# Optimization experiments

Hardware: AMD Instinct MI355X
Metric: run time of the kernel (lower is better)

The kernel has to match this reference:

```python
import jax, jax.numpy as jnp
import numpy as np
import math

DIMS = 2560
N_HEADS = 32
ROT_DIM = 32  # partial rotary (Phi-2)
BASE = 10000.0
B, L = 1, 2048


def apply_rope(x, rot_dim=ROT_DIM, base=BASE, offset=0):
    # x: [B, H, L, hd]; rotate first rot_dim features, pass rest through
    Lx = x.shape[2]
    D = rot_dim // 2
    pos = jnp.arange(offset, offset + Lx, dtype=jnp.float32)              # [L]
    freq = jnp.exp(-jnp.arange(D, dtype=jnp.float32) * (math.log(base) / D))  # [D]
    theta = pos[:, None] * freq[None, :]                                   # [L, D]
    cos, sin = jnp.cos(theta), jnp.sin(theta)
    x1 = x[..., :D]
    x2 = x[..., D:rot_dim]
    rx1 = x1 * cos - x2 * sin
    rx2 = x1 * sin + x2 * cos
    return jnp.concatenate([rx1, rx2, x[..., rot_dim:]], axis=-1)


def setup_inputs() -> dict:
    key = jax.random.key(0)
    k1, k2, k3, k4, k5 = jax.random.split(key, 5)
    x = jax.random.normal(k1, (B, L, DIMS), dtype=jnp.float32)
    Wqkv_w = jax.random.normal(k2, (3 * DIMS, DIMS), dtype=jnp.float32) * 0.02
    Wqkv_b = jax.random.normal(k3, (3 * DIMS,), dtype=jnp.float32) * 0.02
    out_w = jax.random.normal(k4, (DIMS, DIMS), dtype=jnp.float32) * 0.02
    out_b = jax.random.normal(k5, (DIMS,), dtype=jnp.float32) * 0.02
    # additive causal mask, broadcast over batch/heads
    mask = jnp.triu(jnp.full((L, L), -1e9, dtype=jnp.float32), k=1)[None, None]
    return {"x": x, "Wqkv_w": Wqkv_w, "Wqkv_b": Wqkv_b,
            "out_w": out_w, "out_b": out_b, "mask": mask}


def reference(x, Wqkv_w, Wqkv_b, out_w, out_b, mask):
    Bx, Lx, _ = x.shape
    hd = DIMS // N_HEADS  # 80
    qkv = x @ Wqkv_w.T + Wqkv_b                          # [B, L, 3*dims]
    q, k, v = jnp.split(qkv, 3, axis=-1)
    def to_heads(t):
        return t.reshape(Bx, Lx, N_HEADS, hd).transpose(0, 2, 1, 3)  # [B,H,L,hd]
    q, k, v = to_heads(q), to_heads(k), to_heads(v)
    q = apply_rope(q)
    k = apply_rope(k)
    scale = 1.0 / math.sqrt(hd)
    scores = scale * jnp.einsum('bhqd,bhkd->bhqk', q, k) + mask  # [B,H,L,L]
    probs = jax.nn.softmax(scores, axis=-1)
    out = jnp.einsum('bhqk,bhkd->bhqd', probs, v)
    out = out.transpose(0, 2, 1, 3).reshape(Bx, Lx, DIMS)
    return out @ out_w.T + out_b
```

## Files before the change

kernel.cpp:

```cpp
#include <hip/hip_runtime.h>
#include <cstdint>
#include <cmath>

typedef __attribute__((ext_vector_type(4))) float f32x4;
typedef __attribute__((ext_vector_type(8))) short s16x8;

#define LOG2E 1.4426950408889634f

__device__ __forceinline__ unsigned short f2bf(float f) {
    unsigned int u = __float_as_uint(f);
    u += 0x7FFFu + ((u >> 16) & 1u);
    return (unsigned short)(u >> 16);
}
__device__ __forceinline__ float bf2f(unsigned short s) {
    return __uint_as_float(((unsigned int)s) << 16);
}

__device__ __forceinline__ void async_copy16(const void* g, void* l) {
    __builtin_amdgcn_global_load_lds(
        (const __attribute__((address_space(1))) unsigned int*)(uintptr_t)g,
        (__attribute__((address_space(3))) unsigned int*)(uintptr_t)l,
        16, 0, 0);
}

__global__ __launch_bounds__(256) void cast_bf16_kernel(const float* __restrict__ in,
                                                        unsigned short* __restrict__ out,
                                                        int n4) {
    int i = blockIdx.x * 256 + threadIdx.x;
    if (i < n4) {
        float4 v = ((const float4*)in)[i];
        ushort4 o;
        o.x = f2bf(v.x); o.y = f2bf(v.y); o.z = f2bf(v.z); o.w = f2bf(v.w);
        ((ushort4*)out)[i] = o;
    }
}

template <bool BF16_OUT>
__global__ __launch_bounds__(256) void gemm_bt(const unsigned short* __restrict__ A,
                                               const unsigned short* __restrict__ B,
                                               const float* __restrict__ bias,
                                               void* __restrict__ Cout,
                                               int M, int N, int K) {
    __shared__ unsigned short As[128 * 64];
    __shared__ unsigned short Bs[128 * 64];
    const int tid  = threadIdx.x;
    const int lane = tid & 63;
    const int wv   = tid >> 6;
    const int m0 = blockIdx.y * 128;
    const int n0 = blockIdx.x * 128;
    const int w_row = (wv >> 1) * 64;
    const int w_col = (wv & 1) * 64;
    const int fr = lane & 15;
    const int fg = lane >> 4;
    const int srow = lane >> 3;
    const int scol = ((lane & 7) ^ srow) * 8;
    const int rofs0 = ((fg ^ (fr & 7))) * 8;
    const int rofs1 = rofs0 ^ 32;

    f32x4 acc[4][4];
    const f32x4 zf = {0.f, 0.f, 0.f, 0.f};
    for (int r = 0; r < 4; ++r)
        for (int c = 0; c < 4; ++c) acc[r][c] = zf;

    const unsigned short* gA = A + (size_t)(m0 + wv * 32 + srow) * K + scol;
    const unsigned short* gB = B + (size_t)(n0 + wv * 32 + srow) * K + scol;

    for (int k0 = 0; k0 < K; k0 += 64) {
        for (int i = 0; i < 4; ++i)
            async_copy16(gA + (size_t)i * 8 * K + k0, &As[(wv * 32 + i * 8) * 64]);
        for (int i = 0; i < 4; ++i)
            async_copy16(gB + (size_t)i * 8 * K + k0, &Bs[(wv * 32 + i * 8) * 64]);
        __syncthreads();
        {
            s16x8 af[4], bf[4];
            for (int r = 0; r < 4; ++r)
                af[r] = *(const s16x8*)&As[(w_row + r * 16 + fr) * 64 + rofs0];
            for (int c = 0; c < 4; ++c)
                bf[c] = *(const s16x8*)&Bs[(w_col + c * 16 + fr) * 64 + rofs0];
            for (int r = 0; r < 4; ++r)
                for (int c = 0; c < 4; ++c)
                    acc[r][c] = __builtin_amdgcn_mfma_f32_16x16x32_bf16(af[r], bf[c], acc[r][c], 0, 0, 0);
        }
        {
            s16x8 af[4], bf[4];
            for (int r = 0; r < 4; ++r)
                af[r] = *(const s16x8*)&As[(w_row + r * 16 + fr) * 64 + rofs1];
            for (int c = 0; c < 4; ++c)
                bf[c] = *(const s16x8*)&Bs[(w_col + c * 16 + fr) * 64 + rofs1];
            for (int r = 0; r < 4; ++r)
                for (int c = 0; c < 4; ++c)
                    acc[r][c] = __builtin_amdgcn_mfma_f32_16x16x32_bf16(af[r], bf[c], acc[r][c], 0, 0, 0);
        }
        __syncthreads();
    }

    const int rb = (lane >> 4) * 4;
    for (int c = 0; c < 4; ++c) {
        int col = n0 + w_col + c * 16 + fr;
        float bv = bias[col];
        for (int r = 0; r < 4; ++r) {
            int row = m0 + w_row + r * 16 + rb;
            for (int q = 0; q < 4; ++q) {
                float v = acc[r][c][q] + bv;
                if constexpr (BF16_OUT)
                    ((unsigned short*)Cout)[(size_t)(row + q) * N + col] = f2bf(v);
                else
                    ((float*)Cout)[(size_t)(row + q) * N + col] = v;
            }
        }
    }
}


#define BAR()   __builtin_amdgcn_s_barrier()
#define VMW(N)  asm volatile("s_waitcnt vmcnt(" #N ")" ::: "memory")

#define STAGE2(gXb, XsBuf, rb, kk) \
    async_copy16(gXb + (size_t)(rb) * K + (kk), (void*)&XsBuf[(rb) * 64])

#define ST_AS0(b, kk) { STAGE2(gAb, As[b], rbA_0, kk);      STAGE2(gAb, As[b], rbA_1, kk); }
#define ST_AS1(b, kk) { STAGE2(gAb, As[b], rbA_0 + 64, kk); STAGE2(gAb, As[b], rbA_1 + 64, kk); }
#define ST_BS0(b, kk) { STAGE2(gBb, Bs[b], rbB_0, kk);      STAGE2(gBb, Bs[b], rbB_1, kk); }
#define ST_BS1(b, kk) { STAGE2(gBb, Bs[b], rbB_0 + 32, kk); STAGE2(gBb, Bs[b], rbB_1 + 32, kk); }

#define READ_A(b, mh) \
    _Pragma("unroll") \
    for (int mm_ = 0; mm_ < 4; ++mm_) { \
        const unsigned short* ap_ = &As[b][(wr * 128 + (mh) * 64 + mm_ * 16 + fr) * 64]; \
        Ar[mm_][0] = *(const s16x8*)(ap_ + rofs0); \
        Ar[mm_][1] = *(const s16x8*)(ap_ + rofs1); \
    }

#define READ_B(b, nh, Brg) \
    _Pragma("unroll") \
    for (int nn_ = 0; nn_ < 2; ++nn_) { \
        const unsigned short* bp_ = &Bs[b][(wc * 64 + (nh) * 32 + nn_ * 16 + fr) * 64]; \
        Brg[nn_][0] = *(const s16x8*)(bp_ + rofs0); \
        Brg[nn_][1] = *(const s16x8*)(bp_ + rofs1); \
    }

#define MFMA_Q(mh, nh, Brg) \
    _Pragma("unroll") \
    for (int mm_ = 0; mm_ < 4; ++mm_) { \
        _Pragma("unroll") \
        for (int nn_ = 0; nn_ < 2; ++nn_) { \
            acc[(mh) * 4 + mm_][(nh) * 2 + nn_] = __builtin_amdgcn_mfma_f32_16x16x32_bf16( \
                Ar[mm_][0], Brg[nn_][0], acc[(mh) * 4 + mm_][(nh) * 2 + nn_], 0, 0, 0); \
            acc[(mh) * 4 + mm_][(nh) * 2 + nn_] = __builtin_amdgcn_mfma_f32_16x16x32_bf16( \
                Ar[mm_][1], Brg[nn_][1], acc[(mh) * 4 + mm_][(nh) * 2 + nn_], 0, 0, 0); \
        } \
    }

#define GROUP(b, t) { \
    int x1_ = (t) + 1; if (x1_ >= ktiles) x1_ -= ktiles; \
    int x2_ = (t) + 2; if (x2_ >= ktiles) x2_ -= ktiles; \
    const int kn1 = x1_ << 6; \
    const int kn2 = x2_ << 6; \
     \
    __builtin_amdgcn_s_setprio(1); MFMA_Q(0, 0, Br0); __builtin_amdgcn_s_setprio(0); \
    VMW(6); \
    READ_B(b, 1, Br1); \
    ST_AS1((b) ^ 1, kn1); \
    BAR(); \
     \
    __builtin_amdgcn_s_setprio(1); MFMA_Q(0, 1, Br1); __builtin_amdgcn_s_setprio(0); \
    VMW(6); \
    READ_A(b, 1); \
    ST_AS0(b, kn2); \
    BAR(); \
     \
    __builtin_amdgcn_s_setprio(1); MFMA_Q(1, 1, Br1); __builtin_amdgcn_s_setprio(0); \
    VMW(6); \
    ST_BS0(b, kn2); \
    BAR(); \
     \
    __builtin_amdgcn_s_setprio(1); MFMA_Q(1, 0, Br0); __builtin_amdgcn_s_setprio(0); \
    VMW(6); \
    READ_A((b) ^ 1, 0); \
    READ_B((b) ^ 1, 0, Br0); \
    ST_BS1(b, kn2); \
    BAR(); \
}

__global__ __launch_bounds__(512, 2) void gemm256_bt(const unsigned short* __restrict__ A,
                                                     const unsigned short* __restrict__ B,
                                                     const float* __restrict__ bias,
                                                     unsigned short* __restrict__ C,
                                                     int M, int N, int K) {
    __shared__ unsigned short As[2][256 * 64];
    __shared__ unsigned short Bs[2][256 * 64];
    const int tid  = threadIdx.x;
    const int lane = tid & 63;
    const int wv   = tid >> 6;
    const int wr   = wv >> 2;
    const int wc   = wv & 3;
    const int j     = blockIdx.x & 7;
    const int local = blockIdx.x >> 3;
    const int strip = 2 * (j & 3) + (local & 1);
    const int panel = (j >> 2) * 15 + (local >> 1);
    const int m0 = strip * 256;
    const int n0 = panel * 256;
    const int fr = lane & 15;
    const int fg = lane >> 4;
    const int rofs0 = (fg ^ (fr & 7)) * 8;
    const int rofs1 = rofs0 ^ 32;
    const int rlane = lane >> 3;
    const int swzc  = ((lane & 7) ^ (rlane & 7)) * 8;
    const int idx0 = wv * 2, idx1 = wv * 2 + 1;
    const int rbA_0 = idx0 * 8 + ((idx0 >= 8) ? 64 : 0);
    const int rbA_1 = idx1 * 8 + ((idx1 >= 8) ? 64 : 0);
    const int rbB_0 = (idx0 >> 2) * 64 + (idx0 & 3) * 8;
    const int rbB_1 = (idx1 >> 2) * 64 + (idx1 & 3) * 8;
    const int ktiles = K >> 6;

    const unsigned short* gAb = A + (size_t)(m0 + rlane) * K + swzc;
    const unsigned short* gBb = B + (size_t)(n0 + rlane) * K + swzc;

    f32x4 acc[8][4];
    const f32x4 zf = {0.f, 0.f, 0.f, 0.f};
#pragma unroll
    for (int i = 0; i < 8; ++i)
#pragma unroll
        for (int jj = 0; jj < 4; ++jj) acc[i][jj] = zf;

    s16x8 Ar[4][2], Br0[2][2], Br1[2][2];

    ST_AS0(0, 0); ST_AS1(0, 0); ST_BS0(0, 0); ST_BS1(0, 0);
    ST_AS0(1, 64); ST_BS0(1, 64); ST_BS1(1, 64);
    VMW(6);
    BAR();
    READ_A(0, 0);
    READ_B(0, 0, Br0);

    const int nit = ktiles >> 1;
    for (int it = 0; it < nit; ++it) {
        GROUP(0, it * 2);
        GROUP(1, it * 2 + 1);
    }

    const int rb = (lane >> 4) * 4;
#pragma unroll
    for (int nn = 0; nn < 4; ++nn) {
        int col = n0 + wc * 64 + nn * 16 + fr;
        float bv = bias[col];
#pragma unroll
        for (int mm = 0; mm < 8; ++mm) {
            int row = m0 + wr * 128 + mm * 16 + rb;
#pragma unroll
            for (int q = 0; q < 4; ++q) {
                float v = acc[mm][nn][q] + bv;
                C[(size_t)(row + q) * N + col] = f2bf(v);
            }
        }
    }
}

__global__ __launch_bounds__(256) void rope_q_kernel(unsigned short* __restrict__ qkv) {
    int g = blockIdx.x * 256 + threadIdx.x;
    int c = g & 1;
    int h = (g >> 1) & 31;
    int p = g >> 6;
    size_t base = (size_t)p * 7680 + h * 80 + c * 8;
    s16x8 x1v = *(const s16x8*)(qkv + base);
    s16x8 x2v = *(const s16x8*)(qkv + base + 16);
    s16x8 o1, o2;
    for (int j = 0; j < 8; ++j) {
        int dp = c * 8 + j;
        float freq = expf(-(float)dp * 0.57564627324851142f);
        float sn, cs;
        sincosf((float)p * freq, &sn, &cs);
        float x1 = bf2f((unsigned short)x1v[j]);
        float x2 = bf2f((unsigned short)x2v[j]);
        o1[j] = (short)f2bf(x1 * cs - x2 * sn);
        o2[j] = (short)f2bf(x1 * sn + x2 * cs);
    }
    *(s16x8*)(qkv + base)      = o1;
    *(s16x8*)(qkv + base + 16) = o2;
}

__global__ __launch_bounds__(256) void rope_pack_k_kernel(const unsigned short* __restrict__ qkv,
                                                          unsigned short* __restrict__ Kp) {
    int g = blockIdx.x * 256 + threadIdx.x;
    int c   = g % 12;
    int h   = (g / 12) & 31;
    int pos = g / 384;
    int d0 = c * 8;
    const unsigned short* kb = qkv + (size_t)pos * 7680 + 2560 + h * 80;
    s16x8 v = {0, 0, 0, 0, 0, 0, 0, 0};
    if (c >= 4) {
        if (d0 < 80) v = *(const s16x8*)(kb + d0);
    } else if (c < 2) {
        s16x8 x1v = *(const s16x8*)(kb + d0);
        s16x8 x2v = *(const s16x8*)(kb + d0 + 16);
        for (int j = 0; j < 8; ++j) {
            int dp = d0 + j;
            float freq = expf(-(float)dp * 0.57564627324851142f);
            float sn, cs;
            sincosf((float)pos * freq, &sn, &cs);
            v[j] = (short)f2bf(bf2f((unsigned short)x1v[j]) * cs -
                               bf2f((unsigned short)x2v[j]) * sn);
        }
    } else {
        s16x8 x1v = *(const s16x8*)(kb + d0 - 16);
        s16x8 x2v = *(const s16x8*)(kb + d0);
        for (int j = 0; j < 8; ++j) {
            int dp = d0 - 16 + j;
            float freq = expf(-(float)dp * 0.57564627324851142f);
            float sn, cs;
            sincosf((float)pos * freq, &sn, &cs);
            v[j] = (short)f2bf(bf2f((unsigned short)x1v[j]) * sn +
                               bf2f((unsigned short)x2v[j]) * cs);
        }
    }
    *(s16x8*)(Kp + (((size_t)h * 64 + (pos >> 5)) * 12 + c) * 256 + (pos & 31) * 8) = v;
}

__global__ __launch_bounds__(256) void pack_v_kernel(const unsigned short* __restrict__ qkv,
                                                     unsigned short* __restrict__ Vp) {
    int h  = blockIdx.x & 31;
    int g64 = blockIdx.x >> 5;
    int k0 = g64 * 64;
    int tid = threadIdx.x;
    for (int ci = tid; ci < 320; ci += 256) {
        int d   = ci % 80;
        int kbl = ci / 80;
        unsigned short tmp[16];
        for (int j = 0; j < 16; ++j)
            tmp[j] = qkv[(size_t)(k0 + kbl * 16 + j) * 7680 + 5120 + h * 80 + d];
        unsigned short* dst = Vp + ((size_t)h * 128 + g64 * 4 + kbl) * 1280 + d * 16;
        *(s16x8*)dst       = *(const s16x8*)&tmp[0];
        *(s16x8*)(dst + 8) = *(const s16x8*)&tmp[8];
    }
}

__global__ __launch_bounds__(256) void flash6_kernel(const unsigned short* __restrict__ qkv,
                                                     const unsigned short* __restrict__ Kp,
                                                     const unsigned short* __restrict__ Vp,
                                                     unsigned short* __restrict__ attn) {
    __shared__ unsigned short Ks[2][3072];
    __shared__ unsigned short Vs[2][2560];
    __shared__ unsigned short Pt[4][640];
    const int tid  = threadIdx.x;
    const int lane = tid & 63;
    const int wv   = tid >> 6;
    const int h  = blockIdx.x & 31;
    const int jj = blockIdx.x >> 5;
    const int fr = lane & 15;
    const int fg = lane >> 4;
    const float k1 = 0.11180339887498949f * LOG2E;

    const int sA  = jj + 16 * wv;
    const int sB  = jj + 112 - 16 * wv;
    const int smA = sA * 16;
    const int smB = sB * 16;
    const int Ublk = (jj + 114) >> 1;

    const s16x8 zs = {0, 0, 0, 0, 0, 0, 0, 0};
    s16x8 qfA[3], qfB[3];
    {
        const unsigned short* qa = qkv + (size_t)(smA + fr) * 7680 + h * 80;
        const unsigned short* qb = qkv + (size_t)(smB + fr) * 7680 + h * 80;
        for (int sd = 0; sd < 3; ++sd) {
            int d = 32 * sd + fg * 8;
            qfA[sd] = (d < 80) ? *(const s16x8*)(qa + d) : zs;
            qfB[sd] = (d < 80) ? *(const s16x8*)(qb + d) : zs;
        }
    }

    f32x4 OA[5], OB[5];
    const f32x4 zf = {0.f, 0.f, 0.f, 0.f};
    for (int t = 0; t < 5; ++t) { OA[t] = zf; OB[t] = zf; }
    float rsA[4] = {0.f, 0.f, 0.f, 0.f};
    float rsB[4] = {0.f, 0.f, 0.f, 0.f};
    unsigned short* Pw = &Pt[wv][0];

    const unsigned short* Kh = Kp + (size_t)h * 196608;
    const unsigned short* Vh = Vp + (size_t)h * 163840;

#define STG1(q, b, uu) { \
    if ((q) < 6) async_copy16(Kh + (size_t)(uu) * 3072 + (q) * 512 + lane * 8, &Ks[b][(q) * 512]); \
    else         async_copy16(Vh + (size_t)(uu) * 2560 + ((q) - 6) * 512 + lane * 8, &Vs[b][((q) - 6) * 512]); }
#define STAGEU(b, uu) { STG1(wv, b, uu); STG1(wv + 4, b, uu); if (wv < 3) STG1(wv + 8, b, uu); }

#define SMX(SA, RS, SM16, K0, PA) { \
    if ((K0) + 32 > (SM16)) { \
        _Pragma("unroll") \
        for (int g = 0; g < 2; ++g) \
            _Pragma("unroll") \
            for (int r = 0; r < 4; ++r) { \
                int key  = (K0) + g * 16 + fr; \
                int qrow = (SM16) + fg * 4 + r; \
                if (key > qrow) SA[g][r] = -1e30f; \
            } \
    } \
    float pr[2][4]; \
    _Pragma("unroll") \
    for (int g = 0; g < 2; ++g) \
        _Pragma("unroll") \
        for (int r = 0; r < 4; ++r) \
            pr[g][r] = __builtin_amdgcn_exp2f(SA[g][r] * k1); \
    _Pragma("unroll") \
    for (int r = 0; r < 4; ++r) RS[r] += pr[0][r] + pr[1][r]; \
    _Pragma("unroll") \
    for (int g = 0; g < 2; ++g) \
        _Pragma("unroll") \
        for (int r = 0; r < 4; ++r) \
            Pw[(fg * 4 + r) * 40 + g * 16 + fr] = \
                (unsigned short)(__float_as_uint(pr[g][r]) >> 16); \
    PA = *(const s16x8*)(Pw + fr * 40 + fg * 8); }

    STAGEU(0, 0);
    __syncthreads();
    int buf = 0;
    for (int u = 0; u < Ublk; ++u) {
        if (u + 1 < Ublk) STAGEU(buf ^ 1, u + 1);
        const int k0 = u * 32;
        const bool actA = (2 * u <= sA);
        const bool actB = (2 * u <= sB);
        if (actB) {
            s16x8 kb[2][3];
#pragma unroll
            for (int g = 0; g < 2; ++g)
#pragma unroll
                for (int sd = 0; sd < 3; ++sd)
                    kb[g][sd] = *(const s16x8*)&Ks[buf][(fg + sd * 4) * 256 + (g * 16 + fr) * 8];
            s16x8 vb[5];
#pragma unroll
            for (int t = 0; t < 5; ++t)
                vb[t] = *(const s16x8*)&Vs[buf][(fg >> 1) * 1280 + t * 256 + fr * 16 + (fg & 1) * 8];

            f32x4 saA[2] = {zf, zf};
            f32x4 saB[2] = {zf, zf};
            __builtin_amdgcn_s_setprio(1);
            if (actA) {
#pragma unroll
                for (int g = 0; g < 2; ++g)
#pragma unroll
                    for (int sd = 0; sd < 3; ++sd)
                        saA[g] = __builtin_amdgcn_mfma_f32_16x16x32_bf16(qfA[sd], kb[g][sd], saA[g], 0, 0, 0);
            }
#pragma unroll
            for (int g = 0; g < 2; ++g)
#pragma unroll
                for (int sd = 0; sd < 3; ++sd)
                    saB[g] = __builtin_amdgcn_mfma_f32_16x16x32_bf16(qfB[sd], kb[g][sd], saB[g], 0, 0, 0);
            __builtin_amdgcn_s_setprio(0);

            s16x8 paA, paB;
            if (actA) SMX(saA, rsA, smA, k0, paA);
            SMX(saB, rsB, smB, k0, paB);

            __builtin_amdgcn_s_setprio(1);
            if (actA) {
#pragma unroll
                for (int t = 0; t < 5; ++t)
                    OA[t] = __builtin_amdgcn_mfma_f32_16x16x32_bf16(paA, vb[t], OA[t], 0, 0, 0);
            }
#pragma unroll
            for (int t = 0; t < 5; ++t)
                OB[t] = __builtin_amdgcn_mfma_f32_16x16x32_bf16(paB, vb[t], OB[t], 0, 0, 0);
            __builtin_amdgcn_s_setprio(0);
        }
        __syncthreads();
        buf ^= 1;
    }
#undef STG1
#undef STAGEU
#undef SMX

#define FIN6(RS, OO, SM16) { \
    _Pragma("unroll") \
    for (int r = 0; r < 4; ++r) { \
        float v = RS[r]; \
        v += __shfl_xor(v, 1); \
        v += __shfl_xor(v, 2); \
        v += __shfl_xor(v, 4); \
        v += __shfl_xor(v, 8); \
        RS[r] = v; \
    } \
    _Pragma("unroll") \
    for (int r = 0; r < 4; ++r) { \
        float rl = 1.0f / RS[r]; \
        int row = (SM16) + fg * 4 + r; \
        _Pragma("unroll") \
        for (int t = 0; t < 5; ++t) \
            attn[(size_t)row * 2560 + h * 80 + t * 16 + fr] = f2bf(OO[t][r] * rl); \
    } }
    FIN6(rsA, OA, smA);
    FIN6(rsB, OB, smB);
#undef FIN6
}

extern "C" void kernel_launch(void* const* d_in, const int* in_sizes, int n_in,
                              void* d_out, int out_size, void* d_ws, size_t ws_size,
                              hipStream_t stream) {
    const float* x    = (const float*)d_in[0];
    const float* wqkv = (const float*)d_in[1];
    const float* bqkv = (const float*)d_in[2];
    const float* outw = (const float*)d_in[3];
    const float* outb = (const float*)d_in[4];

    unsigned short* xb    = (unsigned short*)d_ws;
    unsigned short* wqkvb = xb + (size_t)2048 * 2560;
    unsigned short* Kp    = wqkvb;
    unsigned short* Vp    = wqkvb + (size_t)32 * 2048 * 96;
    unsigned short* outwb = wqkvb + (size_t)7680 * 2560;
    unsigned short* qkvb  = outwb + (size_t)2560 * 2560;
    unsigned short* attnb = qkvb  + (size_t)2048 * 7680;
    float* out = (float*)d_out;

    cast_bf16_kernel<<<2048 * 2560 / 4 / 256, 256, 0, stream>>>(x, xb, 2048 * 2560 / 4);
    cast_bf16_kernel<<<7680 * 2560 / 4 / 256, 256, 0, stream>>>(wqkv, wqkvb, 7680 * 2560 / 4);
    cast_bf16_kernel<<<2560 * 2560 / 4 / 256, 256, 0, stream>>>(outw, outwb, 2560 * 2560 / 4);

    gemm256_bt<<<240, 512, 0, stream>>>(xb, wqkvb, bqkv, qkvb, 2048, 7680, 2560);

    rope_q_kernel<<<2048 * 64 / 256, 256, 0, stream>>>(qkvb);
    rope_pack_k_kernel<<<2048 * 384 / 256, 256, 0, stream>>>(qkvb, Kp);
    pack_v_kernel<<<32 * 32, 256, 0, stream>>>(qkvb, Vp);

    flash6_kernel<<<512, 256, 0, stream>>>(qkvb, Kp, Vp, attnb);

    gemm_bt<false><<<dim3(2560 / 128, 2048 / 128), 256, 0, stream>>>(
        attnb, outwb, outb, (void*)out, 2048, 2560, 2560);
}
```

Measured before the change: 411.2 us.

## Compute transposed QK^T so P feeds PV MFMA from registers without LDS

The flash attention kernel swaps the MFMA operands so the score tile comes out transposed, with each lane holding consecutive keys for one query row. Probabilities can then be packed straight into the bf16 A-operand register instead of going through a per-wave LDS round trip. The V pack kernel permutes key order within each 32-key block to match the new register layout of P. Row sums collapse to one scalar per lane, reduced with cross-group shuffles at the end. This removes LDS writes and reads and their latency from the inner loop, but it depends on the key permutation exactly matching the MFMA fragment layout.

```diff
diff --git a/kernel.cpp b/kernel.cpp
--- a/kernel.cpp
+++ b/kernel.cpp
@@ -4,6 +4,7 @@
 
 typedef __attribute__((ext_vector_type(4))) float f32x4;
 typedef __attribute__((ext_vector_type(8))) short s16x8;
+typedef __attribute__((ext_vector_type(4))) unsigned int u32x4;
 
 #define LOG2E 1.4426950408889634f
 
@@ -325,21 +326,23 @@
         int d   = ci % 80;
         int kbl = ci / 80;
         unsigned short tmp[16];
-        for (int j = 0; j < 16; ++j)
-            tmp[j] = qkv[(size_t)(k0 + kbl * 16 + j) * 7680 + 5120 + h * 80 + d];
+        for (int j = 0; j < 16; ++j) {
+            int s  = (kbl & 1) * 16 + j;
+            int kt = ((s & 7) >> 2) * 16 + (s >> 3) * 4 + (s & 3);
+            tmp[j] = qkv[(size_t)(k0 + (kbl >> 1) * 32 + kt) * 7680 + 5120 + h * 80 + d];
+        }
         unsigned short* dst = Vp + ((size_t)h * 128 + g64 * 4 + kbl) * 1280 + d * 16;
         *(s16x8*)dst       = *(const s16x8*)&tmp[0];
         *(s16x8*)(dst + 8) = *(const s16x8*)&tmp[8];
     }
 }
 
-__global__ __launch_bounds__(256) void flash6_kernel(const unsigned short* __restrict__ qkv,
+__global__ __launch_bounds__(256) void flash8_kernel(const unsigned short* __restrict__ qkv,
                                                      const unsigned short* __restrict__ Kp,
                                                      const unsigned short* __restrict__ Vp,
                                                      unsigned short* __restrict__ attn) {
     __shared__ unsigned short Ks[2][3072];
     __shared__ unsigned short Vs[2][2560];
-    __shared__ unsigned short Pt[4][640];
     const int tid  = threadIdx.x;
     const int lane = tid & 63;
     const int wv   = tid >> 6;
@@ -370,9 +373,7 @@
     f32x4 OA[5], OB[5];
     const f32x4 zf = {0.f, 0.f, 0.f, 0.f};
     for (int t = 0; t < 5; ++t) { OA[t] = zf; OB[t] = zf; }
-    float rsA[4] = {0.f, 0.f, 0.f, 0.f};
-    float rsB[4] = {0.f, 0.f, 0.f, 0.f};
-    unsigned short* Pw = &Pt[wv][0];
+    float rsA = 0.f, rsB = 0.f;
 
     const unsigned short* Kh = Kp + (size_t)h * 196608;
     const unsigned short* Vh = Vp + (size_t)h * 163840;
@@ -382,14 +383,14 @@
     else         async_copy16(Vh + (size_t)(uu) * 2560 + ((q) - 6) * 512 + lane * 8, &Vs[b][((q) - 6) * 512]); }
 #define STAGEU(b, uu) { STG1(wv, b, uu); STG1(wv + 4, b, uu); if (wv < 3) STG1(wv + 8, b, uu); }
 
-#define SMX(SA, RS, SM16, K0, PA) { \
+#define SMX8(SA, RS, SM16, K0, PA) { \
     if ((K0) + 32 > (SM16)) { \
         _Pragma("unroll") \
         for (int g = 0; g < 2; ++g) \
             _Pragma("unroll") \
             for (int r = 0; r < 4; ++r) { \
-                int key  = (K0) + g * 16 + fr; \
-                int qrow = (SM16) + fg * 4 + r; \
+                int key  = (K0) + g * 16 + fg * 4 + r; \
+                int qrow = (SM16) + fr; \
                 if (key > qrow) SA[g][r] = -1e30f; \
             } \
     } \
@@ -399,15 +400,18 @@
         _Pragma("unroll") \
         for (int r = 0; r < 4; ++r) \
             pr[g][r] = __builtin_amdgcn_exp2f(SA[g][r] * k1); \
-    _Pragma("unroll") \
-    for (int r = 0; r < 4; ++r) RS[r] += pr[0][r] + pr[1][r]; \
+    RS += (pr[0][0] + pr[0][1]) + (pr[0][2] + pr[0][3]) \
+        + (pr[1][0] + pr[1][1]) + (pr[1][2] + pr[1][3]); \
+    u32x4 pw_; \
     _Pragma("unroll") \
     for (int g = 0; g < 2; ++g) \
         _Pragma("unroll") \
-        for (int r = 0; r < 4; ++r) \
-            Pw[(fg * 4 + r) * 40 + g * 16 + fr] = \
-                (unsigned short)(__float_as_uint(pr[g][r]) >> 16); \
-    PA = *(const s16x8*)(Pw + fr * 40 + fg * 8); }
+        for (int q2 = 0; q2 < 2; ++q2) { \
+            unsigned int u0 = __float_as_uint(pr[g][q2 * 2]); \
+            unsigned int u1 = __float_as_uint(pr[g][q2 * 2 + 1]); \
+            pw_[g * 2 + q2] = (u0 >> 16) | (u1 & 0xFFFF0000u); \
+        } \
+    PA = __builtin_bit_cast(s16x8, pw_); }
 
     STAGEU(0, 0);
     __syncthreads();
@@ -437,18 +441,18 @@
                 for (int g = 0; g < 2; ++g)
 #pragma unroll
                     for (int sd = 0; sd < 3; ++sd)
-                        saA[g] = __builtin_amdgcn_mfma_f32_16x16x32_bf16(qfA[sd], kb[g][sd], saA[g], 0, 0, 0);
+                        saA[g] = __builtin_amdgcn_mfma_f32_16x16x32_bf16(kb[g][sd], qfA[sd], saA[g], 0, 0, 0);
             }
 #pragma unroll
             for (int g = 0; g < 2; ++g)
 #pragma unroll
                 for (int sd = 0; sd < 3; ++sd)
-                    saB[g] = __builtin_amdgcn_mfma_f32_16x16x32_bf16(qfB[sd], kb[g][sd], saB[g], 0, 0, 0);
+                    saB[g] = __builtin_amdgcn_mfma_f32_16x16x32_bf16(kb[g][sd], qfB[sd], saB[g], 0, 0, 0);
             __builtin_amdgcn_s_setprio(0);
 
             s16x8 paA, paB;
-            if (actA) SMX(saA, rsA, smA, k0, paA);
-            SMX(saB, rsB, smB, k0, paB);
+            if (actA) SMX8(saA, rsA, smA, k0, paA);
+            SMX8(saB, rsB, smB, k0, paB);
 
             __builtin_amdgcn_s_setprio(1);
             if (actA) {
@@ -466,29 +470,22 @@
     }
 #undef STG1
 #undef STAGEU
-#undef SMX
-
-#define FIN6(RS, OO, SM16) { \
+#undef SMX8
+
+#define FIN8(RS, OO, SM16) { \
+    RS += __shfl_xor(RS, 16); \
+    RS += __shfl_xor(RS, 32); \
     _Pragma("unroll") \
     for (int r = 0; r < 4; ++r) { \
-        float v = RS[r]; \
-        v += __shfl_xor(v, 1); \
-        v += __shfl_xor(v, 2); \
-        v += __shfl_xor(v, 4); \
-        v += __shfl_xor(v, 8); \
-        RS[r] = v; \
-    } \
-    _Pragma("unroll") \
-    for (int r = 0; r < 4; ++r) { \
-        float rl = 1.0f / RS[r]; \
+        float rl = 1.0f / __shfl(RS, fg * 4 + r); \
         int row = (SM16) + fg * 4 + r; \
         _Pragma("unroll") \
         for (int t = 0; t < 5; ++t) \
             attn[(size_t)row * 2560 + h * 80 + t * 16 + fr] = f2bf(OO[t][r] * rl); \
     } }
-    FIN6(rsA, OA, smA);
-    FIN6(rsB, OB, smB);
-#undef FIN6
+    FIN8(rsA, OA, smA);
+    FIN8(rsB, OB, smB);
+#undef FIN8
 }
 
 extern "C" void kernel_launch(void* const* d_in, const int* in_sizes, int n_in,
@@ -519,7 +516,7 @@
     rope_pack_k_kernel<<<2048 * 384 / 256, 256, 0, stream>>>(qkvb, Kp);
     pack_v_kernel<<<32 * 32, 256, 0, stream>>>(qkvb, Vp);
 
-    flash6_kernel<<<512, 256, 0, stream>>>(qkvb, Kp, Vp, attnb);
+    flash8_kernel<<<512, 256, 0, stream>>>(qkvb, Kp, Vp, attnb);
 
     gemm_bt<false><<<dim3(2560 / 128, 2048 / 128), 256, 0, stream>>>(
         attnb, outwb, outb, (void*)out, 2048, 2560, 2560);
```

Result: no change. 407.4 us (-0.9%).
